# Performance work log

Hardware: AMD Instinct MI355X
Metric: run time of the kernel (lower is better)

The kernel has to match this reference:

```python
import jax, jax.numpy as jnp
import numpy as np

N_NODES = 100000
N_EDGES = 1200000
D_IN = 64
D_HID = 64


def _gcn_layer(h_in, W, b, src, dst, norm, n_nodes):
    # h_in: [N, d_in]; W: [d_in, d_out]; norm: [E_total] symmetric deg norm
    h = h_in @ W                                  # [N, d_out]
    msg = h[src] * norm[:, None]                  # gather + scale, [E_total, d_out]
    agg = jax.ops.segment_sum(msg, dst, num_segments=n_nodes)  # scatter-add
    return agg + b


def _prelu(x, a):
    # per-channel PReLU: a broadcasts over nodes
    return jnp.where(x >= 0, x, a * x)


def setup_inputs() -> dict:
    key = jax.random.key(0)
    ks = jax.random.split(key, 8)
    x = jax.random.normal(ks[0], (N_NODES, D_IN), dtype=jnp.float32)
    edge_index = jax.random.randint(ks[1], (2, N_EDGES), 0, N_NODES, dtype=jnp.int64)
    # Glorot-ish weights, PyG GCNConv defaults: weight + bias; PReLU init slope 0.25
    W1 = jax.random.normal(ks[2], (D_IN, D_HID), dtype=jnp.float32) / np.sqrt(D_IN)
    b1 = jnp.zeros((D_HID,), dtype=jnp.float32)
    a1 = jnp.full((D_HID,), 0.25, dtype=jnp.float32)
    W2 = jax.random.normal(ks[3], (D_HID, D_HID), dtype=jnp.float32) / np.sqrt(D_HID)
    b2 = jnp.zeros((D_HID,), dtype=jnp.float32)
    a2 = jnp.full((D_HID,), 0.25, dtype=jnp.float32)
    return {"x": x, "edge_index": edge_index, "W1": W1, "b1": b1, "a1": a1,
            "W2": W2, "b2": b2, "a2": a2}


def reference(x, edge_index, W1, b1, a1, W2, b2, a2):
    n = x.shape[0]
    # add self-loops (GCNConv default add_self_loops=True)
    loops = jnp.arange(n, dtype=edge_index.dtype)
    src = jnp.concatenate([edge_index[0], loops])
    dst = jnp.concatenate([edge_index[1], loops])
    # symmetric normalization: deg computed on destination with unit edge weights
    deg = jax.ops.segment_sum(jnp.ones_like(src, dtype=x.dtype), dst, num_segments=n)
    dinv = jnp.where(deg > 0, jax.lax.rsqrt(deg), 0.0)
    norm = dinv[src] * dinv[dst]                  # [E + N]

    h = _gcn_layer(x, W1, b1, src, dst, norm, n)
    h = _prelu(h, a1)
    h = _gcn_layer(h, W2, b2, src, dst, norm, n)
    h = _prelu(h, a2)
    return h
```

## Files before the change

### kernel.cpp

```cpp
#include <hip/hip_runtime.h>
#include <hip/hip_bf16.h>
#include <hip/hip_fp16.h>

#define D 64
#define NB 256
#define BSHIFT 8
#define NBK 512
#define SUBS 8
#define SCAP 1024
#define CHUNK 8192
#define AGN 32
#define BFSTRIDE 16
#define RECL 4096

typedef _Float16 f16x8 __attribute__((ext_vector_type(8)));
typedef float    f32x4 __attribute__((ext_vector_type(4)));


__global__ void __launch_bounds__(256, 4)
k_bin_gemm(const int* __restrict__ src, const int* __restrict__ dst,
           unsigned* __restrict__ records, int* __restrict__ bucket_fill,
           int E, int nbin,
           const float* __restrict__ X, const float* __restrict__ W,
           __half* __restrict__ H, int n, int ntiles, int gemmb) {
    __shared__ int cnt[NBK];
    __shared__ int gbase[NBK];
    __shared__ _Float16 W1h[D * D];
    __shared__ _Float16 W1s[D * D];
    const int t = threadIdx.x;

    if ((int)blockIdx.x < nbin) {
        const int slot = blockIdx.x & (SUBS - 1);
        cnt[t] = 0; cnt[t + 256] = 0;
        __syncthreads();

        const int base_e = blockIdx.x * CHUNK;
        unsigned rec[32];
        unsigned br[32];
#pragma unroll
        for (int i = 0; i < 8; ++i) {
            const int e0 = base_e + i * 1024 + t * 4;
            if (e0 + 3 < E) {
                int4 s4 = *reinterpret_cast<const int4*>(src + e0);
                int4 d4 = *reinterpret_cast<const int4*>(dst + e0);
                int ss[4] = {s4.x, s4.y, s4.z, s4.w};
                int dd[4] = {d4.x, d4.y, d4.z, d4.w};
#pragma unroll
                for (int j = 0; j < 4; ++j) {
                    int bk = dd[j] >> BSHIFT;
                    rec[i * 4 + j] = ((unsigned)ss[j] << BSHIFT) | (unsigned)(dd[j] & (NB - 1));
                    int rank = atomicAdd(&cnt[bk], 1);
                    br[i * 4 + j] = ((unsigned)bk << 16) | (unsigned)rank;
                }
            } else {
#pragma unroll
                for (int j = 0; j < 4; ++j) {
                    int e = e0 + j;
                    if (e < E) {
                        int s = src[e], d = dst[e];
                        int bk = d >> BSHIFT;
                        rec[i * 4 + j] = ((unsigned)s << BSHIFT) | (unsigned)(d & (NB - 1));
                        int rank = atomicAdd(&cnt[bk], 1);
                        br[i * 4 + j] = ((unsigned)bk << 16) | (unsigned)rank;
                    } else {
                        br[i * 4 + j] = 0xFFFFFFFFu;
                    }
                }
            }
        }
        __syncthreads();
#pragma unroll
        for (int rep = 0; rep < NBK / 256; ++rep) {
            int bk = t + rep * 256;
            if (cnt[bk] > 0)
                gbase[bk] = atomicAdd(&bucket_fill[(bk * SUBS + slot) * BFSTRIDE], cnt[bk]);
        }
        __syncthreads();
#pragma unroll
        for (int i = 0; i < 32; ++i) {
            if (br[i] != 0xFFFFFFFFu) {
                int bk = br[i] >> 16;
                int idx = gbase[bk] + (int)(br[i] & 0xFFFF);
                if (idx < SCAP)
                    records[((size_t)bk * SUBS + slot) * SCAP + idx] = rec[i];
            }
        }
    } else {
        const int lane = t & 63;
        const int wv   = t >> 6;
        const int r16  = lane & 15;
        const int g4   = lane >> 4;

#pragma unroll
        for (int q = 0; q < 4; ++q) {
            float4 wq = *reinterpret_cast<const float4*>(W + t * 16 + q * 4);
            float ws[4] = {wq.x, wq.y, wq.z, wq.w};
#pragma unroll
            for (int m = 0; m < 4; ++m) {
                int widx = t * 16 + q * 4 + m;
                int k   = widx >> 6;
                int col = widx & 63;
                int li  = (((k >> 5) * 4 + ((k >> 3) & 3)) * 64 + col) * 8 + (k & 7);
                _Float16 h = (_Float16)ws[m];
                W1h[li] = h;
                W1s[li] = (_Float16)(ws[m] - (float)h);
            }
        }
        __syncthreads();

        const int gw = (blockIdx.x - nbin) * 4 + wv;
        const int stride = gemmb * 4;
        const int t0 = gw;
        const int t1 = gw + stride;

        auto run_tile = [&](int tile, const float4* xv) {
            float xs[16] = {xv[0].x, xv[0].y, xv[0].z, xv[0].w,
                            xv[1].x, xv[1].y, xv[1].z, xv[1].w,
                            xv[2].x, xv[2].y, xv[2].z, xv[2].w,
                            xv[3].x, xv[3].y, xv[3].z, xv[3].w};
            f16x8 Ah[2], Al[2];
#pragma unroll
            for (int kt = 0; kt < 2; ++kt)
#pragma unroll
                for (int j = 0; j < 8; ++j) {
                    float v = xs[kt * 8 + j];
                    _Float16 h = (_Float16)v;
                    Ah[kt][j] = h;
                    Al[kt][j] = (_Float16)(v - (float)h);
                }
            f32x4 acc[4];
#pragma unroll
            for (int ct = 0; ct < 4; ++ct)
                acc[ct] = (f32x4){0.f, 0.f, 0.f, 0.f};
#pragma unroll
            for (int ct = 0; ct < 4; ++ct) {
#pragma unroll
                for (int kt = 0; kt < 2; ++kt) {
                    int li = ((kt * 4 + g4) * 64 + ct * 16 + r16) * 8;
                    f16x8 Bh = *reinterpret_cast<const f16x8*>(&W1h[li]);
                    f16x8 Bl = *reinterpret_cast<const f16x8*>(&W1s[li]);
                    acc[ct] = __builtin_amdgcn_mfma_f32_16x16x32_f16(Ah[kt], Bh, acc[ct], 0, 0, 0);
                    acc[ct] = __builtin_amdgcn_mfma_f32_16x16x32_f16(Al[kt], Bh, acc[ct], 0, 0, 0);
                    acc[ct] = __builtin_amdgcn_mfma_f32_16x16x32_f16(Ah[kt], Bl, acc[ct], 0, 0, 0);
                }
            }
            const int nb16 = tile * 16;
#pragma unroll
            for (int ct = 0; ct < 4; ++ct)
#pragma unroll
                for (int r = 0; r < 4; ++r) {
                    int node = nb16 + g4 * 4 + r;
                    if (node < n)
                        H[(size_t)node * D + ct * 16 + r16] = __float2half_rn(acc[ct][r]);
                }
        };

        float4 xa[4], xb[4];
        if (t0 < ntiles) {
            int row = t0 * 16 + r16;
            if (row > n - 1) row = n - 1;
            const float* xp = X + (size_t)row * D + g4 * 8;
            xa[0] = *reinterpret_cast<const float4*>(xp);
            xa[1] = *reinterpret_cast<const float4*>(xp + 4);
            xa[2] = *reinterpret_cast<const float4*>(xp + 32);
            xa[3] = *reinterpret_cast<const float4*>(xp + 36);
        }
        if (t1 < ntiles) {
            int row = t1 * 16 + r16;
            if (row > n - 1) row = n - 1;
            const float* xp = X + (size_t)row * D + g4 * 8;
            xb[0] = *reinterpret_cast<const float4*>(xp);
            xb[1] = *reinterpret_cast<const float4*>(xp + 4);
            xb[2] = *reinterpret_cast<const float4*>(xp + 32);
            xb[3] = *reinterpret_cast<const float4*>(xp + 36);
        }
        if (t0 < ntiles) run_tile(t0, xa);
        if (t1 < ntiles) run_tile(t1, xb);
    }
}


__global__ void __launch_bounds__(512)
k_csr(const unsigned* __restrict__ records,
      const int* __restrict__ bucket_fill,
      int* __restrict__ edge_base,
      int* __restrict__ rowbeg, int* __restrict__ rowcnt,
      float* __restrict__ dinv,
      int* __restrict__ csr_src, int n) {
    __shared__ unsigned recl[RECL];
    __shared__ int stage[RECL];
    __shared__ int cnt[NB];
    __shared__ int excl[NB];
    __shared__ int wsum[4];
    __shared__ int sbase;

    const int t = threadIdx.x;
    const int b = blockIdx.x;
    const int lane = t & 63;

    int subcnt[SUBS], soff[SUBS];
    int cnt_e = 0;
#pragma unroll
    for (int s = 0; s < SUBS; ++s) {
        subcnt[s] = bucket_fill[(b * SUBS + s) * BFSTRIDE];
        soff[s] = cnt_e;
        cnt_e += subcnt[s];
    }
    if (cnt_e > RECL) cnt_e = RECL;

    if (t < NB) cnt[t] = 0;

#pragma unroll
    for (int s = 0; s < SUBS; ++s) {
        const size_t so = ((size_t)b * SUBS + s) * SCAP;
        const int off = soff[s];
        for (int i = t; i < subcnt[s]; i += 512)
            if (off + i < RECL)
                recl[off + i] = records[so + i];
    }
    __syncthreads();

    for (int i = t; i < cnt_e; i += 512)
        atomicAdd(&cnt[recl[i] & (NB - 1)], 1);
    __syncthreads();

    int c0 = 0, v = 0;
    if (t < NB) {
        c0 = cnt[t];
        v = c0;
#pragma unroll
        for (int off = 1; off < 64; off <<= 1) {
            int u = __shfl_up(v, off, 64);
            if (lane >= off) v += u;
        }
        if (lane == 63) wsum[t >> 6] = v;
    }
    if (t == 0) sbase = atomicAdd(edge_base, cnt_e);
    __syncthreads();
    if (t < NB) {
        int pre = 0;
#pragma unroll
        for (int w = 0; w < 4; ++w)
            if (w < (t >> 6)) pre += wsum[w];
        const int ex = v + pre - c0;
        excl[t] = ex;
        int node = b * NB + t;
        if (node < n) {
            rowbeg[node] = sbase + ex;
            rowcnt[node] = c0;
            dinv[node]   = rsqrtf((float)(c0 + 1));
        }
        cnt[t] = 0;
    }
    __syncthreads();

    for (int i = t; i < cnt_e; i += 512) {
        unsigned r = recl[i];
        int d8 = r & (NB - 1);
        int rank = atomicAdd(&cnt[d8], 1);
        stage[excl[d8] + rank] = (int)(r >> BSHIFT);
    }
    __syncthreads();

    const int base = sbase;
    for (int i = t; i < cnt_e; i += 512)
        csr_src[base + i] = stage[i];
}

__device__ __forceinline__ void edge_accum(const __half* __restrict__ Hn,
                                           const int* __restrict__ csr_src,
                                           int beg, int end, int part, float acc[8]) {
    int idx[8];
#pragma unroll
    for (int j = 0; j < 8; ++j)
        idx[j] = (beg + j < end) ? csr_src[beg + j] : 0;
    int k = beg;
    while (k < end) {
        int s[8];
        float w[8];
#pragma unroll
        for (int j = 0; j < 8; ++j) {
            s[j] = idx[j];
            w[j] = (k + j < end) ? 1.f : 0.f;
        }
        int kn = k + 8;
#pragma unroll
        for (int j = 0; j < 8; ++j)
            idx[j] = (kn + j < end) ? csr_src[kn + j] : 0;
        uint4 g[8];
#pragma unroll
        for (int j = 0; j < 8; ++j)
            g[j] = *reinterpret_cast<const uint4*>(Hn + (size_t)s[j] * D + part);
#pragma unroll
        for (int j = 0; j < 8; ++j) {
            const __half2* p = reinterpret_cast<const __half2*>(&g[j]);
#pragma unroll
            for (int i = 0; i < 4; ++i) {
                float2 f = __half22float2(p[i]);
                acc[2 * i + 0] += w[j] * f.x;
                acc[2 * i + 1] += w[j] * f.y;
            }
        }
        k = kn;
    }
}

__device__ __forceinline__ void edge_accum_sc(const __half* __restrict__ Hn,
                                              const int* __restrict__ csr_src,
                                              const float* __restrict__ dinv,
                                              int beg, int end, int part, float acc[8]) {
    int idx[8];
    float dv[8];
#pragma unroll
    for (int j = 0; j < 8; ++j)
        idx[j] = (beg + j < end) ? csr_src[beg + j] : 0;
#pragma unroll
    for (int j = 0; j < 8; ++j)
        dv[j] = dinv[idx[j]];
    int k = beg;
    while (k < end) {
        int s[8];
        float w[8];
#pragma unroll
        for (int j = 0; j < 8; ++j) {
            s[j] = idx[j];
            w[j] = (k + j < end) ? dv[j] : 0.f;
        }
        int kn = k + 8;
#pragma unroll
        for (int j = 0; j < 8; ++j)
            idx[j] = (kn + j < end) ? csr_src[kn + j] : 0;
#pragma unroll
        for (int j = 0; j < 8; ++j)
            dv[j] = dinv[idx[j]];
        uint4 g[8];
#pragma unroll
        for (int j = 0; j < 8; ++j)
            g[j] = *reinterpret_cast<const uint4*>(Hn + (size_t)s[j] * D + part);
#pragma unroll
        for (int j = 0; j < 8; ++j) {
            const __half2* p = reinterpret_cast<const __half2*>(&g[j]);
#pragma unroll
            for (int i = 0; i < 4; ++i) {
                float2 f = __half22float2(p[i]);
                acc[2 * i + 0] += w[j] * f.x;
                acc[2 * i + 1] += w[j] * f.y;
            }
        }
        k = kn;
    }
}


__global__ void __launch_bounds__(256, 5)
k_agg_gemm(const __half* __restrict__ Hn1,
           const int* __restrict__ rowbeg,
           const int* __restrict__ rowcnt,
           const int* __restrict__ csr_src,
           const float* __restrict__ dinv,
           const float* __restrict__ b1, const float* __restrict__ a1,
           const float* __restrict__ W2,
           __half* __restrict__ Hn2, int n) {
    __shared__ _Float16 W2h[D * D];
    __shared__ _Float16 W2s[D * D];
    __shared__ float Yl[AGN][68];

    const int t = threadIdx.x;

#pragma unroll
    for (int q = 0; q < 4; ++q) {
        float4 wq = *reinterpret_cast<const float4*>(W2 + t * 16 + q * 4);
        float ws[4] = {wq.x, wq.y, wq.z, wq.w};
#pragma unroll
        for (int m = 0; m < 4; ++m) {
            int widx = t * 16 + q * 4 + m;
            int k   = widx >> 6;
            int col = widx & 63;
            int li  = (((k >> 5) * 4 + ((k >> 3) & 3)) * 64 + col) * 8 + (k & 7);
            _Float16 h = (_Float16)ws[m];
            W2h[li] = h;
            W2s[li] = (_Float16)(ws[m] - (float)h);
        }
    }

    const int nl   = t >> 3;
    const int part = (t & 7) * 8;
    const int node = blockIdx.x * AGN + nl;

    if (node < n) {
        float di = dinv[node];
        float acc[8];
        {
            uint4 g = *reinterpret_cast<const uint4*>(Hn1 + (size_t)node * D + part);
            const __half2* p = reinterpret_cast<const __half2*>(&g);
#pragma unroll
            for (int i = 0; i < 4; ++i) {
                float2 f = __half22float2(p[i]);
                acc[2 * i + 0] = f.x * di;
                acc[2 * i + 1] = f.y * di;
            }
        }
        const int beg = rowbeg[node];
        edge_accum_sc(Hn1, csr_src, dinv, beg, beg + rowcnt[node], part, acc);

        const float4 b0 = *reinterpret_cast<const float4*>(b1 + part);
        const float4 b4 = *reinterpret_cast<const float4*>(b1 + part + 4);
        const float4 a0 = *reinterpret_cast<const float4*>(a1 + part);
        const float4 a4 = *reinterpret_cast<const float4*>(a1 + part + 4);
        float y0 = acc[0] * di + b0.x, y1 = acc[1] * di + b0.y;
        float y2 = acc[2] * di + b0.z, y3 = acc[3] * di + b0.w;
        float y4 = acc[4] * di + b4.x, y5 = acc[5] * di + b4.y;
        float y6 = acc[6] * di + b4.z, y7 = acc[7] * di + b4.w;
        Yl[nl][part + 0] = (y0 >= 0.f) ? y0 : a0.x * y0;
        Yl[nl][part + 1] = (y1 >= 0.f) ? y1 : a0.y * y1;
        Yl[nl][part + 2] = (y2 >= 0.f) ? y2 : a0.z * y2;
        Yl[nl][part + 3] = (y3 >= 0.f) ? y3 : a0.w * y3;
        Yl[nl][part + 4] = (y4 >= 0.f) ? y4 : a4.x * y4;
        Yl[nl][part + 5] = (y5 >= 0.f) ? y5 : a4.y * y5;
        Yl[nl][part + 6] = (y6 >= 0.f) ? y6 : a4.z * y6;
        Yl[nl][part + 7] = (y7 >= 0.f) ? y7 : a4.w * y7;
        if ((t & 7) == 0) Yl[nl][64] = di;
    }
    __syncthreads();

    {
        const int lane = t & 63;
        const int wvq  = t >> 6;
        const int r16  = lane & 15;
        const int g4   = lane >> 4;
        const int rt   = wvq >> 1;
        const int cp   = wvq & 1;

        f32x4 acc2[2];
        acc2[0] = (f32x4){0.f, 0.f, 0.f, 0.f};
        acc2[1] = (f32x4){0.f, 0.f, 0.f, 0.f};
#pragma unroll
        for (int kt = 0; kt < 2; ++kt) {
            const float* yp = &Yl[rt * 16 + r16][kt * 32 + g4 * 8];
            f16x8 Ah, Al;
#pragma unroll
            for (int j = 0; j < 8; ++j) {
                float v = yp[j];
                _Float16 h = (_Float16)v;
                Ah[j] = h;
                Al[j] = (_Float16)(v - (float)h);
            }
#pragma unroll
            for (int ci = 0; ci < 2; ++ci) {
                int li = ((kt * 4 + g4) * 64 + (cp * 2 + ci) * 16 + r16) * 8;
                f16x8 Bh = *reinterpret_cast<const f16x8*>(&W2h[li]);
                f16x8 Bl = *reinterpret_cast<const f16x8*>(&W2s[li]);
                acc2[ci] = __builtin_amdgcn_mfma_f32_16x16x32_f16(Ah, Bh, acc2[ci], 0, 0, 0);
                acc2[ci] = __builtin_amdgcn_mfma_f32_16x16x32_f16(Al, Bh, acc2[ci], 0, 0, 0);
                acc2[ci] = __builtin_amdgcn_mfma_f32_16x16x32_f16(Ah, Bl, acc2[ci], 0, 0, 0);
            }
        }
#pragma unroll
        for (int ci = 0; ci < 2; ++ci)
#pragma unroll
            for (int r = 0; r < 4; ++r) {
                int row = rt * 16 + g4 * 4 + r;
                int nd  = blockIdx.x * AGN + row;
                if (nd < n) {
                    float dr = Yl[row][64];
                    Hn2[(size_t)nd * D + (cp * 2 + ci) * 16 + r16] =
                        __float2half_rn(acc2[ci][r] * dr);
                }
            }
    }
}


__global__ void k_aggregate(const __half* __restrict__ Hn,
                            const int* __restrict__ rowbeg,
                            const int* __restrict__ rowcnt,
                            const int* __restrict__ csr_src,
                            const float* __restrict__ dinv,
                            const float* __restrict__ b, const float* __restrict__ a,
                            float* __restrict__ out, int n) {
    int t = blockIdx.x * blockDim.x + threadIdx.x;
    int node = t >> 3;
    if (node >= n) return;
    int part = (t & 7) * 8;

    float di = dinv[node];
    float acc[8];
    {
        uint4 g = *reinterpret_cast<const uint4*>(Hn + (size_t)node * D + part);
        const __half2* p = reinterpret_cast<const __half2*>(&g);
#pragma unroll
        for (int i = 0; i < 4; ++i) {
            float2 f = __half22float2(p[i]);
            acc[2 * i + 0] = f.x;
            acc[2 * i + 1] = f.y;
        }
    }
    const int beg = rowbeg[node];
    edge_accum(Hn, csr_src, beg, beg + rowcnt[node], part, acc);

    const float4 b0 = *reinterpret_cast<const float4*>(b + part);
    const float4 b4 = *reinterpret_cast<const float4*>(b + part + 4);
    const float4 a0 = *reinterpret_cast<const float4*>(a + part);
    const float4 a4 = *reinterpret_cast<const float4*>(a + part + 4);
    float4 r0, r1;
    r0.x = acc[0] * di + b0.x; r0.y = acc[1] * di + b0.y;
    r0.z = acc[2] * di + b0.z; r0.w = acc[3] * di + b0.w;
    r1.x = acc[4] * di + b4.x; r1.y = acc[5] * di + b4.y;
    r1.z = acc[6] * di + b4.z; r1.w = acc[7] * di + b4.w;
    r0.x = (r0.x >= 0.f) ? r0.x : a0.x * r0.x;
    r0.y = (r0.y >= 0.f) ? r0.y : a0.y * r0.y;
    r0.z = (r0.z >= 0.f) ? r0.z : a0.z * r0.z;
    r0.w = (r0.w >= 0.f) ? r0.w : a0.w * r0.w;
    r1.x = (r1.x >= 0.f) ? r1.x : a4.x * r1.x;
    r1.y = (r1.y >= 0.f) ? r1.y : a4.y * r1.y;
    r1.z = (r1.z >= 0.f) ? r1.z : a4.z * r1.z;
    r1.w = (r1.w >= 0.f) ? r1.w : a4.w * r1.w;
    float* o = out + (size_t)node * D + part;
    *reinterpret_cast<float4*>(o) = r0;
    *reinterpret_cast<float4*>(o + 4) = r1;
}

extern "C" void kernel_launch(void* const* d_in, const int* in_sizes, int n_in,
                              void* d_out, int out_size, void* d_ws, size_t ws_size,
                              hipStream_t stream) {
    const float* x  = (const float*)d_in[0];
    const int*   ei = (const int*)  d_in[1];
    const float* W1 = (const float*)d_in[2];
    const float* b1 = (const float*)d_in[3];
    const float* a1 = (const float*)d_in[4];
    const float* W2 = (const float*)d_in[5];
    const float* b2 = (const float*)d_in[6];
    const float* a2 = (const float*)d_in[7];
    float* out = (float*)d_out;

    const int n   = in_sizes[0] / D;
    const int E   = in_sizes[1] / 2;
    const int n64 = n * D;

    const int* src = ei;
    const int* dst = ei + E;

    const int nbuckets = (n + NB - 1) >> BSHIFT;

    int*      bucket_fill = (int*)d_ws;
    int*      edge_base   = bucket_fill + 60000;
    unsigned* records     = (unsigned*)(bucket_fill + 4096 * BFSTRIDE);
    int*      rowbeg      = (int*)(records + (size_t)nbuckets * SUBS * SCAP);
    int*      rowcnt      = rowbeg + ((n + 256) & ~255);
    float*    dinv        = (float*)(rowcnt + ((n + 256) & ~255));
    int*      csr_src     = (int*)(dinv + ((n + 256) & ~255));
    __half*   Hn1         = (__half*)(csr_src + ((E + 255) & ~255));
    __half*   Hn2         = Hn1 + (((size_t)n64 + 256) & ~(size_t)255);

    const int B = 256;
    const int nbin   = (E + CHUNK - 1) / CHUNK;
    const int ntiles = (n + 15) / 16;
    const int gemmb  = 782;

    hipMemsetAsync(bucket_fill, 0, 4096 * BFSTRIDE * sizeof(int), stream);

    k_bin_gemm<<<nbin + gemmb, B, 0, stream>>>(src, dst, records, bucket_fill, E, nbin,
                                               x, W1, Hn1, n, ntiles, gemmb);
    k_csr<<<nbuckets, 512, 0, stream>>>(records, bucket_fill, edge_base,
                                        rowbeg, rowcnt, dinv, csr_src, n);
    k_agg_gemm<<<(n + AGN - 1) / AGN, B, 0, stream>>>(Hn1, rowbeg, rowcnt, csr_src, dinv,
                                                      b1, a1, W2, Hn2, n);
    k_aggregate<<<(n * 8 + B - 1) / B, B, 0, stream>>>(Hn2, rowbeg, rowcnt, csr_src, dinv,
                                                       b2, a2, out, n);
}
```

Measured before the change: 174.3 us.

## Sort nodes by in-degree within buckets to balance aggregation waves

```diff
diff --git a/kernel.cpp b/kernel.cpp
--- a/kernel.cpp
+++ b/kernel.cpp
@@ -185,6 +185,7 @@
       const int* __restrict__ bucket_fill,
       int* __restrict__ edge_base,
       int* __restrict__ rowbeg, int* __restrict__ rowcnt,
+      int* __restrict__ perm,
       float* __restrict__ dinv,
       int* __restrict__ csr_src, int n) {
     __shared__ unsigned recl[RECL];
@@ -193,6 +194,8 @@
     __shared__ int excl[NB];
     __shared__ int wsum[4];
     __shared__ int sbase;
+    __shared__ int dcnt[64];
+    __shared__ int dbase[64];
 
     const int t = threadIdx.x;
     const int b = blockIdx.x;
@@ -209,6 +212,7 @@
     if (cnt_e > RECL) cnt_e = RECL;
 
     if (t < NB) cnt[t] = 0;
+    if (t < 64) dcnt[t] = 0;
 
 #pragma unroll
     for (int s = 0; s < SUBS; ++s) {
@@ -224,9 +228,11 @@
         atomicAdd(&cnt[recl[i] & (NB - 1)], 1);
     __syncthreads();
 
-    int c0 = 0, v = 0;
+    int c0 = 0, v = 0, dcl = 0;
     if (t < NB) {
         c0 = cnt[t];
+        dcl = (c0 < 63) ? c0 : 63;
+        atomicAdd(&dcnt[dcl], 1);
         v = c0;
 #pragma unroll
         for (int off = 1; off < 64; off <<= 1) {
@@ -237,6 +243,17 @@
     }
     if (t == 0) sbase = atomicAdd(edge_base, cnt_e);
     __syncthreads();
+    if (t < 64) {
+        int dv = dcnt[t];
+        int sv = dv;
+#pragma unroll
+        for (int off = 1; off < 64; off <<= 1) {
+            int u = __shfl_up(sv, off, 64);
+            if (lane >= off) sv += u;
+        }
+        dbase[t] = sv - dv;
+        dcnt[t] = 0;
+    }
     if (t < NB) {
         int pre = 0;
 #pragma unroll
@@ -254,6 +271,10 @@
     }
     __syncthreads();
 
+    if (t < NB) {
+        int r = atomicAdd(&dcnt[dcl], 1);
+        perm[b * NB + dbase[dcl] + r] = b * NB + t;
+    }
     for (int i = t; i < cnt_e; i += 512) {
         unsigned r = recl[i];
         int d8 = r & (NB - 1);
@@ -357,6 +378,7 @@
            const int* __restrict__ rowbeg,
            const int* __restrict__ rowcnt,
            const int* __restrict__ csr_src,
+           const int* __restrict__ perm,
            const float* __restrict__ dinv,
            const float* __restrict__ b1, const float* __restrict__ a1,
            const float* __restrict__ W2,
@@ -364,6 +386,7 @@
     __shared__ _Float16 W2h[D * D];
     __shared__ _Float16 W2s[D * D];
     __shared__ float Yl[AGN][68];
+    __shared__ int pnode[AGN];
 
     const int t = threadIdx.x;
 
@@ -385,7 +408,8 @@
 
     const int nl   = t >> 3;
     const int part = (t & 7) * 8;
-    const int node = blockIdx.x * AGN + nl;
+    const int node = perm[blockIdx.x * AGN + nl];
+    if ((t & 7) == 0) pnode[nl] = node;
 
     if (node < n) {
         float di = dinv[node];
@@ -420,6 +444,10 @@
         Yl[nl][part + 6] = (y6 >= 0.f) ? y6 : a4.z * y6;
         Yl[nl][part + 7] = (y7 >= 0.f) ? y7 : a4.w * y7;
         if ((t & 7) == 0) Yl[nl][64] = di;
+    } else {
+#pragma unroll
+        for (int i = 0; i < 8; ++i) Yl[nl][part + i] = 0.f;
+        if ((t & 7) == 0) Yl[nl][64] = 0.f;
     }
     __syncthreads();
 
@@ -460,7 +488,7 @@
 #pragma unroll
             for (int r = 0; r < 4; ++r) {
                 int row = rt * 16 + g4 * 4 + r;
-                int nd  = blockIdx.x * AGN + row;
+                int nd  = pnode[row];
                 if (nd < n) {
                     float dr = Yl[row][64];
                     Hn2[(size_t)nd * D + (cp * 2 + ci) * 16 + r16] =
@@ -475,11 +503,12 @@
                             const int* __restrict__ rowbeg,
                             const int* __restrict__ rowcnt,
                             const int* __restrict__ csr_src,
+                            const int* __restrict__ perm,
                             const float* __restrict__ dinv,
                             const float* __restrict__ b, const float* __restrict__ a,
                             float* __restrict__ out, int n) {
     int t = blockIdx.x * blockDim.x + threadIdx.x;
-    int node = t >> 3;
+    int node = perm[t >> 3];
     if (node >= n) return;
     int part = (t & 7) * 8;
 
@@ -541,14 +570,16 @@
     const int* dst = ei + E;
 
     const int nbuckets = (n + NB - 1) >> BSHIFT;
+    const int npad     = nbuckets * NB;
 
     int*      bucket_fill = (int*)d_ws;
     int*      edge_base   = bucket_fill + 60000;
     unsigned* records     = (unsigned*)(bucket_fill + 4096 * BFSTRIDE);
     int*      rowbeg      = (int*)(records + (size_t)nbuckets * SUBS * SCAP);
-    int*      rowcnt      = rowbeg + ((n + 256) & ~255);
-    float*    dinv        = (float*)(rowcnt + ((n + 256) & ~255));
-    int*      csr_src     = (int*)(dinv + ((n + 256) & ~255));
+    int*      rowcnt      = rowbeg + npad;
+    int*      perm        = rowcnt + npad;
+    float*    dinv        = (float*)(perm + npad);
+    int*      csr_src     = (int*)(dinv + npad);
     __half*   Hn1         = (__half*)(csr_src + ((E + 255) & ~255));
     __half*   Hn2         = Hn1 + (((size_t)n64 + 256) & ~(size_t)255);
 
@@ -562,9 +593,9 @@
     k_bin_gemm<<<nbin + gemmb, B, 0, stream>>>(src, dst, records, bucket_fill, E, nbin,
                                                x, W1, Hn1, n, ntiles, gemmb);
     k_csr<<<nbuckets, 512, 0, stream>>>(records, bucket_fill, edge_base,
-                                        rowbeg, rowcnt, dinv, csr_src, n);
-    k_agg_gemm<<<(n + AGN - 1) / AGN, B, 0, stream>>>(Hn1, rowbeg, rowcnt, csr_src, dinv,
-                                                      b1, a1, W2, Hn2, n);
-    k_aggregate<<<(n * 8 + B - 1) / B, B, 0, stream>>>(Hn2, rowbeg, rowcnt, csr_src, dinv,
-                                                       b2, a2, out, n);
+                                        rowbeg, rowcnt, perm, dinv, csr_src, n);
+    k_agg_gemm<<<npad / AGN, B, 0, stream>>>(Hn1, rowbeg, rowcnt, csr_src, perm, dinv,
+                                             b1, a1, W2, Hn2, n);
+    k_aggregate<<<npad * 8 / B, B, 0, stream>>>(Hn2, rowbeg, rowcnt, csr_src, perm, dinv,
+                                                b2, a2, out, n);
 }
```

New measurement: 188.0 us. 1.08x slower.
